# Kernel tuning notes

Measured on AMD Instinct MI355X. Metric: run time of the kernel, lower is better.

Reference implementation:

```python
import jax, jax.numpy as jnp
import numpy as np

B, NUM_FRAMES, NUM_PATCHES = 2, 16, 196
DIM, H, DH = 768, 12, 64
T = NUM_FRAMES * NUM_PATCHES  # 3136
EPS = 1e-5


def setup_inputs() -> dict:
    key = jax.random.key(0)
    ks = jax.random.split(key, 5)
    x = jax.random.normal(ks[0], (B, T, DIM), jnp.float32)
    context = jax.random.normal(ks[1], (B, T, DIM), jnp.float32)
    Wq = jax.random.normal(ks[2], (DIM, H * DH), jnp.float32) * 0.02
    Wkv = jax.random.normal(ks[3], (DIM, 2 * H * DH), jnp.float32) * 0.02
    Wo = jax.random.normal(ks[4], (H * DH, DIM), jnp.float32) * 0.02
    bo = jnp.zeros((DIM,), jnp.float32)
    gamma = jnp.ones((DIM,), jnp.float32)
    beta = jnp.zeros((DIM,), jnp.float32)
    # block-diagonal frame mask: patch i attends to patch j iff same frame
    frame_ids = jnp.arange(T) // NUM_PATCHES
    mask = frame_ids[:, None] == frame_ids[None, :]  # [T, T] bool
    return {"x": x, "context": context, "Wq": Wq, "Wkv": Wkv, "Wo": Wo,
            "bo": bo, "gamma": gamma, "beta": beta, "mask": mask}


def reference(x, context, Wq, Wkv, Wo, bo, gamma, beta, mask):
    # LayerNorm on queries only (torch LN: biased variance, eps=1e-5)
    mu = jnp.mean(x, axis=-1, keepdims=True)
    var = jnp.var(x, axis=-1, keepdims=True)
    xn = (x - mu) * jax.lax.rsqrt(var + EPS) * gamma + beta

    q = xn @ Wq                      # [B, T, H*DH]
    kv = context @ Wkv               # [B, T, 2*H*DH]
    k, v = jnp.split(kv, 2, axis=-1)

    def split_heads(t):
        return t.reshape(B, T, H, DH).transpose(0, 2, 1, 3)  # [B, H, T, DH]

    q, k, v = split_heads(q), split_heads(k), split_heads(v)

    scale = DH ** -0.5
    dots = jnp.einsum('bhnd,bhmd->bhnm', q, k) * scale      # [B, H, T, T]
    dots = jnp.where(mask, dots, -jnp.inf)
    attn = jax.nn.softmax(dots, axis=-1)                    # dropout p=0.0 -> identity
    out = jnp.einsum('bhnm,bhmd->bhnd', attn, v)            # [B, H, T, DH]
    out = out.transpose(0, 2, 1, 3).reshape(B, T, H * DH)
    return out @ Wo + bo
```

## Files before the change

### kernel.cpp

```cpp
#include <hip/hip_runtime.h>
#include <hip/hip_bf16.h>

#define NB 2
#define TT 3136
#define DIM 768
#define NH 12
#define NF 16
#define NP 196

typedef __attribute__((ext_vector_type(8))) short short8;
typedef __attribute__((ext_vector_type(4))) short s16x4;
typedef __attribute__((ext_vector_type(4))) float f32x4;
typedef unsigned int uint;

__device__ __forceinline__ float bf2f(short s) {
    return __uint_as_float(((uint)(unsigned short)s) << 16);
}
__device__ __forceinline__ short f2bs(float f) {
    __hip_bfloat16 h = __float2bfloat16(f);
    short s; __builtin_memcpy(&s, &h, 2); return s;
}
__device__ __forceinline__ uint pack2bf(float a, float b) {
    return (uint)(unsigned short)f2bs(a) | ((uint)(unsigned short)f2bs(b) << 16);
}
__device__ __forceinline__ void load16_lds(const void* g, void* l) {
    __builtin_amdgcn_global_load_lds(
        (const __attribute__((address_space(1))) unsigned int*)g,
        (__attribute__((address_space(3))) unsigned int*)l, 16, 0, 0);
}

__global__ __launch_bounds__(256)
void prep_all(const float* __restrict__ Wq, const float* __restrict__ Wkv,
              const float* __restrict__ Wo,
              __hip_bfloat16* __restrict__ WqT, __hip_bfloat16* __restrict__ WkvT,
              __hip_bfloat16* __restrict__ WoT,
              const float* __restrict__ ctx, __hip_bfloat16* __restrict__ cb,
              const float* __restrict__ x, const float* __restrict__ gamma,
              const float* __restrict__ beta, __hip_bfloat16* __restrict__ xn) {
    __shared__ float tile[32][33];
    int blk = blockIdx.x, tid = threadIdx.x;
    if (blk < 2304) {
        int bx = blk % 96, ky = blk / 96;
        const float* W; __hip_bfloat16* WT; int N, n0;
        if (bx < 24)      { W = Wq;  WT = WqT;  N = DIM;     n0 = bx * 32; }
        else if (bx < 72) { W = Wkv; WT = WkvT; N = 2 * DIM; n0 = (bx - 24) * 32; }
        else              { W = Wo;  WT = WoT;  N = DIM;     n0 = (bx - 72) * 32; }
        int k0 = ky * 32;
        int tx = tid & 31, ty = tid >> 5;
#pragma unroll
        for (int i = 0; i < 32; i += 8)
            tile[ty + i][tx] = W[(size_t)(k0 + ty + i) * N + (n0 + tx)];
        __syncthreads();
#pragma unroll
        for (int i = 0; i < 32; i += 8)
            WT[(size_t)(n0 + ty + i) * DIM + (k0 + tx)] = __float2bfloat16(tile[tx][ty + i]);
        return;
    }
    blk -= 2304;
    if (blk < 4704) {
        size_t i = (size_t)blk * 256 + tid;
        f32x4 f; __builtin_memcpy(&f, ctx + i * 4, 16);
        s16x4 s;
#pragma unroll
        for (int j = 0; j < 4; j++) s[j] = f2bs(f[j]);
        __builtin_memcpy((short*)cb + i * 4, &s, 8);
        return;
    }
    blk -= 4704;
    int wave = tid >> 6, lane = tid & 63;
    int row = blk * 4 + wave;
    const float* xr = x + (size_t)row * DIM;
    f32x4 v[3];
    float s = 0.f, ss = 0.f;
#pragma unroll
    for (int i = 0; i < 3; i++) {
        __builtin_memcpy(&v[i], xr + lane * 4 + i * 256, 16);
#pragma unroll
        for (int j = 0; j < 4; j++) { s += v[i][j]; ss += v[i][j] * v[i][j]; }
    }
#pragma unroll
    for (int off = 32; off; off >>= 1) {
        s += __shfl_xor(s, off);
        ss += __shfl_xor(ss, off);
    }
    float mu = s / DIM;
    float rs = rsqrtf(ss / DIM - mu * mu + 1e-5f);
#pragma unroll
    for (int i = 0; i < 3; i++) {
        int c = lane * 4 + i * 256;
        f32x4 g, bt;
        __builtin_memcpy(&g, gamma + c, 16);
        __builtin_memcpy(&bt, beta + c, 16);
        s16x4 o;
#pragma unroll
        for (int j = 0; j < 4; j++) o[j] = f2bs((v[i][j] - mu) * rs * g[j] + bt[j]);
        __builtin_memcpy((short*)xn + (size_t)row * DIM + c, &o, 8);
    }
}

__global__ __launch_bounds__(512, 1)
void gemm_qkv(const __hip_bfloat16* __restrict__ xn,
              const __hip_bfloat16* __restrict__ cb,
              const __hip_bfloat16* __restrict__ WqT,
              const __hip_bfloat16* __restrict__ WkvT,
              __hip_bfloat16* __restrict__ qbuf,
              __hip_bfloat16* __restrict__ kvbuf) {
    __shared__ short lds[3][24576];

    int orig = blockIdx.x;
    int xcd = orig & 7, pos = orig >> 3;
    int wgid = (xcd < 1 ? xcd * 56 : 56 + (xcd - 1) * 55) + pos;
    int mt = wgid / 9, nt = wgid - mt * 9;

    const __hip_bfloat16 *Abase, *Bbase; __hip_bfloat16* Cbase;
    int N, n0;
    if (nt < 3) { Abase = xn; Bbase = WqT;  Cbase = qbuf;  N = DIM;  n0 = nt * 256; }
    else        { Abase = cb; Bbase = WkvT; Cbase = kvbuf; N = 1536; n0 = (nt - 3) * 256; }
    int m0 = mt * 128;

    int tid = threadIdx.x, lane = tid & 63, wave = tid >> 6;
    int r = lane & 15, q = lane >> 4;
    int wm = wave >> 2, wn = wave & 3;
    f32x4 acc[4][4] = {};

    auto stageT = [&](int buf, int kt) {
        int k0 = kt * 64;
#pragma unroll
        for (int s = 0; s < 2; s++) {
            int idx = s * 512 + tid;
            int row = idx >> 3, cg = idx & 7;
            int w = (cg << 4) ^ ((row & 7) << 4);
            load16_lds((const char*)Abase + ((size_t)(m0 + row) * DIM + k0) * 2 + w,
                       (char*)&lds[buf][0] + idx * 16);
        }
#pragma unroll
        for (int h = 0; h < 2; h++)
#pragma unroll
            for (int s = 0; s < 2; s++) {
                int idx = s * 512 + tid;
                int row = idx >> 3, cg = idx & 7;
                int w = (cg << 4) ^ ((row & 7) << 4);
                load16_lds((const char*)Bbase + ((size_t)(n0 + h * 128 + row) * DIM + k0) * 2 + w,
                           (char*)&lds[buf][8192 + h * 8192] + idx * 16);
            }
    };

    auto read_frag = [&](const char* base, int frag_row, int ks) {
        short8 v;
        int byte_ = frag_row * 128 + ((ks * 64 + q * 16) ^ ((r & 7) << 4));
        __builtin_memcpy(&v, base + byte_, 16);
        return v;
    };

    auto compute = [&](int buf) {
        const char* Ab = (const char*)&lds[buf][0];
        const char* Bb = (const char*)&lds[buf][8192 + (wn >> 1) * 8192];
        int brow0 = (wn & 1) * 64;
        short8 af[4][2], bf[4][2];
#pragma unroll
        for (int m = 0; m < 4; m++)
#pragma unroll
            for (int ks = 0; ks < 2; ks++)
                af[m][ks] = read_frag(Ab, wm * 64 + m * 16 + r, ks);
#pragma unroll
        for (int n = 0; n < 4; n++)
#pragma unroll
            for (int ks = 0; ks < 2; ks++)
                bf[n][ks] = read_frag(Bb, brow0 + n * 16 + r, ks);
        __builtin_amdgcn_s_setprio(1);
#pragma unroll
        for (int m = 0; m < 4; m++)
#pragma unroll
            for (int n = 0; n < 4; n++)
#pragma unroll
                for (int ks = 0; ks < 2; ks++)
                    acc[m][n] = __builtin_amdgcn_mfma_f32_16x16x32_bf16(
                        af[m][ks], bf[n][ks], acc[m][n], 0, 0, 0);
        __builtin_amdgcn_s_setprio(0);
    };

    stageT(0, 0); stageT(1, 1);
    asm volatile("s_waitcnt vmcnt(6)" ::: "memory");
    __builtin_amdgcn_s_barrier();

    for (int t = 0; t < 12; ++t) {
        if (t < 10) stageT((t + 2) % 3, t + 2);
        compute(t % 3);
        if (t < 10)       asm volatile("s_waitcnt vmcnt(6)" ::: "memory");
        else if (t == 10) asm volatile("s_waitcnt vmcnt(0)" ::: "memory");
        if (t < 11) __builtin_amdgcn_s_barrier();
    }

#pragma unroll
    for (int m = 0; m < 4; m++)
#pragma unroll
        for (int n = 0; n < 4; n++)
#pragma unroll
            for (int rr = 0; rr < 4; rr++) {
                int row = m0 + wm * 64 + m * 16 + q * 4 + rr;
                int col = n0 + wn * 64 + n * 16 + r;
                Cbase[(size_t)row * N + col] = __float2bfloat16(acc[m][n][rr]);
            }
}

__global__ __launch_bounds__(256)
void gemm_o(const __hip_bfloat16* __restrict__ A,
            const __hip_bfloat16* __restrict__ BT,
            const float* __restrict__ bias,
            float* __restrict__ C) {
    __shared__ short sA[2][128 * 64];
    __shared__ short sB[2][128 * 64];
    int orig = blockIdx.x;
    int xcd = orig & 7, pos = orig >> 3;
    int wgid = (xcd < 6 ? xcd * 37 : 222 + (xcd - 6) * 36) + pos;
    int mt = wgid / 6, nt = wgid - mt * 6;
    int m0 = mt * 128, n0 = nt * 128;
    int tid = threadIdx.x, lane = tid & 63, wave = tid >> 6;
    int r = lane & 15, q = lane >> 4;
    int wm = (wave & 1) * 64, wn = (wave >> 1) * 64;
    f32x4 acc[4][4] = {};

    auto stage = [&](int buf, int k0) {
#pragma unroll
        for (int i = 0; i < 4; i++) {
            int c = i * 256 + tid;
            int row = c >> 3, cg = c & 7;
            load16_lds(A + (size_t)(m0 + row) * DIM + k0 + cg * 8, &sA[buf][c * 8]);
        }
#pragma unroll
        for (int i = 0; i < 4; i++) {
            int c = i * 256 + tid;
            int row = c >> 3, cg = c & 7;
            load16_lds(BT + (size_t)(n0 + row) * DIM + k0 + cg * 8, &sB[buf][c * 8]);
        }
    };
    auto compute = [&](int buf) {
#pragma unroll
        for (int ks = 0; ks < 2; ks++) {
            short8 af[4], bfv[4];
#pragma unroll
            for (int t = 0; t < 4; t++) {
                __builtin_memcpy(&af[t],  &sA[buf][(wm + t * 16 + r) * 64 + ks * 32 + q * 8], 16);
                __builtin_memcpy(&bfv[t], &sB[buf][(wn + t * 16 + r) * 64 + ks * 32 + q * 8], 16);
            }
            __builtin_amdgcn_s_setprio(1);
#pragma unroll
            for (int mi = 0; mi < 4; mi++)
#pragma unroll
                for (int ni = 0; ni < 4; ni++)
                    acc[mi][ni] = __builtin_amdgcn_mfma_f32_16x16x32_bf16(
                        af[mi], bfv[ni], acc[mi][ni], 0, 0, 0);
            __builtin_amdgcn_s_setprio(0);
        }
    };

    stage(0, 0);
    __syncthreads();
    int cur = 0;
#pragma unroll 2
    for (int t = 0; t < 11; ++t) {
        stage(cur ^ 1, (t + 1) * 64);
        compute(cur);
        __syncthreads();
        cur ^= 1;
    }
    compute(cur);

    float bv[4];
#pragma unroll
    for (int ni = 0; ni < 4; ni++) bv[ni] = bias[n0 + wn + ni * 16 + r];
#pragma unroll
    for (int mi = 0; mi < 4; mi++)
#pragma unroll
        for (int ni = 0; ni < 4; ni++)
#pragma unroll
            for (int rr = 0; rr < 4; rr++) {
                int row = m0 + wm + mi * 16 + q * 4 + rr;
                int col = n0 + wn + ni * 16 + r;
                C[(size_t)row * DIM + col] = acc[mi][ni][rr] + bv[ni];
            }
}

__global__ __launch_bounds__(448, 4)
void attn_kernel(__hip_bfloat16* qo,
                 const __hip_bfloat16* __restrict__ kvb) {
    __shared__ short sK[208 * 66];
    __shared__ short sVT[64 * 226];
    int blk = blockIdx.x;
    int f = blk % NF, h = (blk / NF) % NH, b = blk / (NF * NH);
    size_t tok0 = (size_t)b * TT + (size_t)f * NP;
    int tid = threadIdx.x, wave = tid >> 6, lane = tid & 63;
    int r = lane & 15, q = lane >> 4;

    short8 qf[2][2];
#pragma unroll
    for (int half = 0; half < 2; half++) {
        int qrow = half * 98 + wave * 16 + r;
        if (qrow >= NP) qrow = 0;
        const __hip_bfloat16* src = qo + (tok0 + qrow) * DIM + h * 64;
        __builtin_memcpy(&qf[half][0], src + q * 8, 16);
        __builtin_memcpy(&qf[half][1], src + 32 + q * 8, 16);
    }

    for (int e = tid; e < 1664; e += 448) {
        int row = e >> 3, cg = e & 7;
        short8 t = {0,0,0,0,0,0,0,0};
        if (row < NP)
            __builtin_memcpy(&t, kvb + (tok0 + row) * 1536 + h * 64 + cg * 8, 16);
        __builtin_memcpy(&sK[row * 66 + cg * 8], &t, 16);
    }
    for (int jj = 0; jj < 224; jj += 28) {
        int j = jj + (tid >> 4);
        int d = (tid & 15) * 4;
        s16x4 v = {0, 0, 0, 0};
        if (j < NP)
            __builtin_memcpy(&v, kvb + (tok0 + j) * 1536 + DIM + h * 64 + d, 8);
#pragma unroll
        for (int i = 0; i < 4; i++) sVT[(d + i) * 226 + j] = v[i];
    }
    __syncthreads();

#pragma unroll
    for (int half = 0; half < 2; half++) {
        int row0 = half * 98;

        f32x4 sacc[13];
#pragma unroll
        for (int jf = 0; jf < 13; jf++) {
            f32x4 a = {};
            short8 kf;
            __builtin_memcpy(&kf, &sK[(jf * 16 + r) * 66 + q * 8], 16);
            a = __builtin_amdgcn_mfma_f32_16x16x32_bf16(kf, qf[half][0], a, 0, 0, 0);
            __builtin_memcpy(&kf, &sK[(jf * 16 + r) * 66 + 32 + q * 8], 16);
            a = __builtin_amdgcn_mfma_f32_16x16x32_bf16(kf, qf[half][1], a, 0, 0, 0);
            sacc[jf] = a;
        }

        const float scale = 0.125f;
        float mx = -INFINITY;
#pragma unroll
        for (int jf = 0; jf < 13; jf++)
#pragma unroll
            for (int rg = 0; rg < 4; rg++) {
                bool valid = (jf < 12) | (q == 0);
                if (valid) mx = fmaxf(mx, sacc[jf][rg] * scale);
            }
        mx = fmaxf(mx, __shfl_xor(mx, 16));
        mx = fmaxf(mx, __shfl_xor(mx, 32));
        float ps = 0.f;
#pragma unroll
        for (int jf = 0; jf < 13; jf++)
#pragma unroll
            for (int rg = 0; rg < 4; rg++) {
                bool valid = (jf < 12) | (q == 0);
                float p = valid ? __expf(sacc[jf][rg] * scale - mx) : 0.f;
                sacc[jf][rg] = p;
                ps += p;
            }
        ps += __shfl_xor(ps, 16);
        ps += __shfl_xor(ps, 32);
        float inv = 1.f / ps;

        uint pk01[13], pk23[13];
#pragma unroll
        for (int jf = 0; jf < 13; jf++) {
            pk01[jf] = pack2bf(sacc[jf][0] * inv, sacc[jf][1] * inv);
            pk23[jf] = pack2bf(sacc[jf][2] * inv, sacc[jf][3] * inv);
        }
        int sl = (((2 * q) & 3) << 4) | r;
        int sh = (((2 * q + 1) & 3) << 4) | r;
        bool hiq = q >= 2;
        short8 pa[7];
#pragma unroll
        for (int c = 0; c < 7; c++) {
            uint a0 = (uint)__shfl((int)pk01[2 * c], sl, 64);
            uint a1 = (uint)__shfl((int)pk23[2 * c], sl, 64);
            uint a2 = (uint)__shfl((int)pk01[2 * c], sh, 64);
            uint a3 = (uint)__shfl((int)pk23[2 * c], sh, 64);
            uint b0 = 0, b1 = 0, b2 = 0, b3 = 0;
            if (c < 6) {
                b0 = (uint)__shfl((int)pk01[2 * c + 1], sl, 64);
                b1 = (uint)__shfl((int)pk23[2 * c + 1], sl, 64);
                b2 = (uint)__shfl((int)pk01[2 * c + 1], sh, 64);
                b3 = (uint)__shfl((int)pk23[2 * c + 1], sh, 64);
            }
            uint w[4] = { hiq ? b0 : a0, hiq ? b1 : a1, hiq ? b2 : a2, hiq ? b3 : a3 };
            __builtin_memcpy(&pa[c], w, 16);
        }

#pragma unroll
        for (int nt = 0; nt < 4; nt++) {
            f32x4 oacc = {};
#pragma unroll
            for (int kc = 0; kc < 7; kc++) {
                short8 bfv;
                __builtin_memcpy(&bfv, &sVT[(nt * 16 + r) * 226 + kc * 32 + q * 8], 16);
                oacc = __builtin_amdgcn_mfma_f32_16x16x32_bf16(pa[kc], bfv, oacc, 0, 0, 0);
            }
#pragma unroll
            for (int rg = 0; rg < 4; rg++) {
                int local = wave * 16 + q * 4 + rg;
                if (local < 98)
                    qo[(tok0 + row0 + local) * DIM + h * 64 + nt * 16 + r] =
                        __float2bfloat16(oacc[rg]);
            }
        }
    }
}

extern "C" void kernel_launch(void* const* d_in, const int* in_sizes, int n_in,
                              void* d_out, int out_size, void* d_ws, size_t ws_size,
                              hipStream_t stream) {
    const float* x     = (const float*)d_in[0];
    const float* ctx   = (const float*)d_in[1];
    const float* Wq    = (const float*)d_in[2];
    const float* Wkv   = (const float*)d_in[3];
    const float* Wo    = (const float*)d_in[4];
    const float* bo    = (const float*)d_in[5];
    const float* gamma = (const float*)d_in[6];
    const float* beta  = (const float*)d_in[7];

    char* ws = (char*)d_ws;
    __hip_bfloat16* cbuf  = (__hip_bfloat16*)(ws + 0);
    __hip_bfloat16* kvbuf = (__hip_bfloat16*)(ws + 9633792);
    __hip_bfloat16* qbuf  = (__hip_bfloat16*)(ws + 28901376);
    __hip_bfloat16* WqT   = (__hip_bfloat16*)(ws + 38535168);
    __hip_bfloat16* WkvT  = (__hip_bfloat16*)(ws + 39714816);
    __hip_bfloat16* WoT   = (__hip_bfloat16*)(ws + 42074112);
    __hip_bfloat16* xnbuf = (__hip_bfloat16*)d_out;
    float*          out   = (float*)d_out;

    prep_all<<<8576, 256, 0, stream>>>(Wq, Wkv, Wo, WqT, WkvT, WoT,
                                       ctx, cbuf, x, gamma, beta, xnbuf);
    gemm_qkv<<<441, 512, 0, stream>>>(xnbuf, cbuf, WqT, WkvT, qbuf, kvbuf);
    attn_kernel<<<NB * NH * NF, 448, 0, stream>>>(qbuf, kvbuf);
    gemm_o<<<294, 256, 0, stream>>>(qbuf, WoT, bo, out);
}
```

Measured before the change: 205.7 us.

## Fuse K/V projection into attention kernel and shrink QKV GEMM to Q-only

```diff
diff --git a/kernel.cpp b/kernel.cpp
--- a/kernel.cpp
+++ b/kernel.cpp
@@ -98,108 +98,77 @@
     }
 }
 
-__global__ __launch_bounds__(512, 1)
-void gemm_qkv(const __hip_bfloat16* __restrict__ xn,
-              const __hip_bfloat16* __restrict__ cb,
-              const __hip_bfloat16* __restrict__ WqT,
-              const __hip_bfloat16* __restrict__ WkvT,
-              __hip_bfloat16* __restrict__ qbuf,
-              __hip_bfloat16* __restrict__ kvbuf) {
-    __shared__ short lds[3][24576];
-
+__global__ __launch_bounds__(256)
+void gemm_q(const __hip_bfloat16* __restrict__ A,
+            const __hip_bfloat16* __restrict__ BT,
+            __hip_bfloat16* __restrict__ C) {
+    __shared__ short sA[2][128 * 64];
+    __shared__ short sB[2][128 * 64];
     int orig = blockIdx.x;
     int xcd = orig & 7, pos = orig >> 3;
-    int wgid = (xcd < 1 ? xcd * 56 : 56 + (xcd - 1) * 55) + pos;
-    int mt = wgid / 9, nt = wgid - mt * 9;
-
-    const __hip_bfloat16 *Abase, *Bbase; __hip_bfloat16* Cbase;
-    int N, n0;
-    if (nt < 3) { Abase = xn; Bbase = WqT;  Cbase = qbuf;  N = DIM;  n0 = nt * 256; }
-    else        { Abase = cb; Bbase = WkvT; Cbase = kvbuf; N = 1536; n0 = (nt - 3) * 256; }
-    int m0 = mt * 128;
-
+    int wgid = (xcd < 6 ? xcd * 37 : 222 + (xcd - 6) * 36) + pos;
+    int mt = wgid / 6, nt = wgid - mt * 6;
+    int m0 = mt * 128, n0 = nt * 128;
     int tid = threadIdx.x, lane = tid & 63, wave = tid >> 6;
     int r = lane & 15, q = lane >> 4;
-    int wm = wave >> 2, wn = wave & 3;
+    int wm = (wave & 1) * 64, wn = (wave >> 1) * 64;
     f32x4 acc[4][4] = {};
 
-    auto stageT = [&](int buf, int kt) {
-        int k0 = kt * 64;
-#pragma unroll
-        for (int s = 0; s < 2; s++) {
-            int idx = s * 512 + tid;
-            int row = idx >> 3, cg = idx & 7;
-            int w = (cg << 4) ^ ((row & 7) << 4);
-            load16_lds((const char*)Abase + ((size_t)(m0 + row) * DIM + k0) * 2 + w,
-                       (char*)&lds[buf][0] + idx * 16);
-        }
-#pragma unroll
-        for (int h = 0; h < 2; h++)
-#pragma unroll
-            for (int s = 0; s < 2; s++) {
-                int idx = s * 512 + tid;
-                int row = idx >> 3, cg = idx & 7;
-                int w = (cg << 4) ^ ((row & 7) << 4);
-                load16_lds((const char*)Bbase + ((size_t)(n0 + h * 128 + row) * DIM + k0) * 2 + w,
-                           (char*)&lds[buf][8192 + h * 8192] + idx * 16);
-            }
+    auto stage = [&](int buf, int k0) {
+#pragma unroll
+        for (int i = 0; i < 4; i++) {
+            int c = i * 256 + tid;
+            int row = c >> 3, cg = c & 7;
+            load16_lds(A + (size_t)(m0 + row) * DIM + k0 + cg * 8, &sA[buf][c * 8]);
+        }
+#pragma unroll
+        for (int i = 0; i < 4; i++) {
+            int c = i * 256 + tid;
+            int row = c >> 3, cg = c & 7;
+            load16_lds(BT + (size_t)(n0 + row) * DIM + k0 + cg * 8, &sB[buf][c * 8]);
+        }
     };
-
-    auto read_frag = [&](const char* base, int frag_row, int ks) {
-        short8 v;
-        int byte_ = frag_row * 128 + ((ks * 64 + q * 16) ^ ((r & 7) << 4));
-        __builtin_memcpy(&v, base + byte_, 16);
-        return v;
+    auto compute = [&](int buf) {
+#pragma unroll
+        for (int ks = 0; ks < 2; ks++) {
+            short8 af[4], bfv[4];
+#pragma unroll
+            for (int t = 0; t < 4; t++) {
+                __builtin_memcpy(&af[t],  &sA[buf][(wm + t * 16 + r) * 64 + ks * 32 + q * 8], 16);
+                __builtin_memcpy(&bfv[t], &sB[buf][(wn + t * 16 + r) * 64 + ks * 32 + q * 8], 16);
+            }
+            __builtin_amdgcn_s_setprio(1);
+#pragma unroll
+            for (int mi = 0; mi < 4; mi++)
+#pragma unroll
+                for (int ni = 0; ni < 4; ni++)
+                    acc[mi][ni] = __builtin_amdgcn_mfma_f32_16x16x32_bf16(
+                        af[mi], bfv[ni], acc[mi][ni], 0, 0, 0);
+            __builtin_amdgcn_s_setprio(0);
+        }
     };
 
-    auto compute = [&](int buf) {
-        const char* Ab = (const char*)&lds[buf][0];
-        const char* Bb = (const char*)&lds[buf][8192 + (wn >> 1) * 8192];
-        int brow0 = (wn & 1) * 64;
-        short8 af[4][2], bf[4][2];
-#pragma unroll
-        for (int m = 0; m < 4; m++)
-#pragma unroll
-            for (int ks = 0; ks < 2; ks++)
-                af[m][ks] = read_frag(Ab, wm * 64 + m * 16 + r, ks);
-#pragma unroll
-        for (int n = 0; n < 4; n++)
-#pragma unroll
-            for (int ks = 0; ks < 2; ks++)
-                bf[n][ks] = read_frag(Bb, brow0 + n * 16 + r, ks);
-        __builtin_amdgcn_s_setprio(1);
-#pragma unroll
-        for (int m = 0; m < 4; m++)
-#pragma unroll
-            for (int n = 0; n < 4; n++)
-#pragma unroll
-                for (int ks = 0; ks < 2; ks++)
-                    acc[m][n] = __builtin_amdgcn_mfma_f32_16x16x32_bf16(
-                        af[m][ks], bf[n][ks], acc[m][n], 0, 0, 0);
-        __builtin_amdgcn_s_setprio(0);
-    };
-
-    stageT(0, 0); stageT(1, 1);
-    asm volatile("s_waitcnt vmcnt(6)" ::: "memory");
-    __builtin_amdgcn_s_barrier();
-
-    for (int t = 0; t < 12; ++t) {
-        if (t < 10) stageT((t + 2) % 3, t + 2);
-        compute(t % 3);
-        if (t < 10)       asm volatile("s_waitcnt vmcnt(6)" ::: "memory");
-        else if (t == 10) asm volatile("s_waitcnt vmcnt(0)" ::: "memory");
-        if (t < 11) __builtin_amdgcn_s_barrier();
-    }
-
-#pragma unroll
-    for (int m = 0; m < 4; m++)
-#pragma unroll
-        for (int n = 0; n < 4; n++)
+    stage(0, 0);
+    __syncthreads();
+    int cur = 0;
+#pragma unroll 2
+    for (int t = 0; t < 11; ++t) {
+        stage(cur ^ 1, (t + 1) * 64);
+        compute(cur);
+        __syncthreads();
+        cur ^= 1;
+    }
+    compute(cur);
+
+#pragma unroll
+    for (int mi = 0; mi < 4; mi++)
+#pragma unroll
+        for (int ni = 0; ni < 4; ni++)
 #pragma unroll
             for (int rr = 0; rr < 4; rr++) {
-                int row = m0 + wm * 64 + m * 16 + q * 4 + rr;
-                int col = n0 + wn * 64 + n * 16 + r;
-                Cbase[(size_t)row * N + col] = __float2bfloat16(acc[m][n][rr]);
+                int row = m0 + wm + mi * 16 + q * 4 + rr;
+                int col = n0 + wn + ni * 16 + r;
+                C[(size_t)row * DIM + col] = __float2bfloat16(acc[mi][ni][rr]);
             }
 }
 
@@ -283,9 +252,13 @@
 
 __global__ __launch_bounds__(448, 4)
 void attn_kernel(__hip_bfloat16* qo,
-                 const __hip_bfloat16* __restrict__ kvb) {
-    __shared__ short sK[208 * 66];
-    __shared__ short sVT[64 * 226];
+                 const __hip_bfloat16* __restrict__ cb,
+                 const __hip_bfloat16* __restrict__ WkvT) {
+    __shared__ short smem[28192];
+    short* cbS = smem;
+    short* wS  = smem + 12544;
+    short* sK  = smem;
+    short* sVT = smem + 13728;
     int blk = blockIdx.x;
     int f = blk % NF, h = (blk / NF) % NH, b = blk / (NF * NH);
     size_t tok0 = (size_t)b * TT + (size_t)f * NP;
@@ -302,21 +275,69 @@
         __builtin_memcpy(&qf[half][1], src + 32 + q * 8, 16);
     }
 
-    for (int e = tid; e < 1664; e += 448) {
-        int row = e >> 3, cg = e & 7;
-        short8 t = {0,0,0,0,0,0,0,0};
-        if (row < NP)
-            __builtin_memcpy(&t, kvb + (tok0 + row) * 1536 + h * 64 + cg * 8, 16);
-        __builtin_memcpy(&sK[row * 66 + cg * 8], &t, 16);
-    }
-    for (int jj = 0; jj < 224; jj += 28) {
-        int j = jj + (tid >> 4);
-        int d = (tid & 15) * 4;
-        s16x4 v = {0, 0, 0, 0};
-        if (j < NP)
-            __builtin_memcpy(&v, kvb + (tok0 + j) * 1536 + DIM + h * 64 + d, 8);
-#pragma unroll
-        for (int i = 0; i < 4; i++) sVT[(d + i) * 226 + j] = v[i];
+    f32x4 acc0[8] = {}, acc1[8] = {};
+    for (int kc = 0; kc < 12; kc++) {
+        if (kc) __syncthreads();
+        int k0 = kc * 64;
+        for (int e = tid; e < 1568; e += 448) {
+            int row = e >> 3, cg = e & 7;
+            int sw = (cg ^ (row & 7)) << 4;
+            load16_lds((const char*)cb + ((size_t)(tok0 + row) * DIM + k0) * 2 + sw,
+                       (char*)cbS + e * 16);
+        }
+        for (int e = tid; e < 1024; e += 448) {
+            int row = e >> 3, cg = e & 7;
+            int sw = (cg ^ (row & 7)) << 4;
+            int wrow = (row < 64) ? (h * 64 + row) : (DIM + h * 64 + row - 64);
+            load16_lds((const char*)WkvT + ((size_t)wrow * DIM + k0) * 2 + sw,
+                       (char*)wS + e * 16);
+        }
+        __syncthreads();
+
+        short8 a0[2], a1[2];
+#pragma unroll
+        for (int ks = 0; ks < 2; ks++) {
+            int b0 = (2 * wave * 16 + r) * 128 + ((ks * 64 + q * 16) ^ ((r & 7) << 4));
+            int b1 = ((2 * wave + 1) * 16 + r) * 128 + ((ks * 64 + q * 16) ^ ((r & 7) << 4));
+            __builtin_memcpy(&a0[ks], (char*)cbS + b0, 16);
+            __builtin_memcpy(&a1[ks], (char*)cbS + b1, 16);
+        }
+        __builtin_amdgcn_s_setprio(1);
+#pragma unroll
+        for (int df = 0; df < 8; df++)
+#pragma unroll
+            for (int ks = 0; ks < 2; ks++) {
+                short8 bfv;
+                int bb = (df * 16 + r) * 128 + ((ks * 64 + q * 16) ^ ((r & 7) << 4));
+                __builtin_memcpy(&bfv, (char*)wS + bb, 16);
+                acc0[df] = __builtin_amdgcn_mfma_f32_16x16x32_bf16(a0[ks], bfv, acc0[df], 0, 0, 0);
+                acc1[df] = __builtin_amdgcn_mfma_f32_16x16x32_bf16(a1[ks], bfv, acc1[df], 0, 0, 0);
+            }
+        __builtin_amdgcn_s_setprio(0);
+    }
+    __syncthreads();
+
+#pragma unroll
+    for (int jj = 0; jj < 2; jj++)
+#pragma unroll
+        for (int df = 0; df < 8; df++)
+#pragma unroll
+            for (int i = 0; i < 4; i++) {
+                int j = (2 * wave + jj) * 16 + q * 4 + i;
+                if (j < NP) {
+                    float v = jj ? acc1[df][i] : acc0[df][i];
+                    short s = f2bs(v);
+                    if (df < 4) sK[j * 66 + df * 16 + r] = s;
+                    else        sVT[(df * 16 + r - 64) * 226 + j] = s;
+                }
+            }
+    for (int e = tid; e < 12 * 66; e += 448) {
+        int row = NP + e / 66, c = e % 66;
+        sK[row * 66 + c] = 0;
+    }
+    for (int e = tid; e < 64 * 30; e += 448) {
+        int d = e / 30, j = NP + e % 30;
+        sVT[d * 226 + j] = 0;
     }
     __syncthreads();
 
@@ -422,17 +443,16 @@
 
     char* ws = (char*)d_ws;
     __hip_bfloat16* cbuf  = (__hip_bfloat16*)(ws + 0);
-    __hip_bfloat16* kvbuf = (__hip_bfloat16*)(ws + 9633792);
-    __hip_bfloat16* qbuf  = (__hip_bfloat16*)(ws + 28901376);
-    __hip_bfloat16* WqT   = (__hip_bfloat16*)(ws + 38535168);
-    __hip_bfloat16* WkvT  = (__hip_bfloat16*)(ws + 39714816);
-    __hip_bfloat16* WoT   = (__hip_bfloat16*)(ws + 42074112);
+    __hip_bfloat16* qbuf  = (__hip_bfloat16*)(ws + 9633792);
+    __hip_bfloat16* WqT   = (__hip_bfloat16*)(ws + 19267584);
+    __hip_bfloat16* WkvT  = (__hip_bfloat16*)(ws + 20447232);
+    __hip_bfloat16* WoT   = (__hip_bfloat16*)(ws + 22806528);
     __hip_bfloat16* xnbuf = (__hip_bfloat16*)d_out;
     float*          out   = (float*)d_out;
 
     prep_all<<<8576, 256, 0, stream>>>(Wq, Wkv, Wo, WqT, WkvT, WoT,
                                        ctx, cbuf, x, gamma, beta, xnbuf);
-    gemm_qkv<<<441, 512, 0, stream>>>(xnbuf, cbuf, WqT, WkvT, qbuf, kvbuf);
-    attn_kernel<<<NB * NH * NF, 448, 0, stream>>>(qbuf, kvbuf);
+    gemm_q<<<294, 256, 0, stream>>>(xnbuf, WqT, qbuf);
+    attn_kernel<<<NB * NH * NF, 448, 0, stream>>>(qbuf, cbuf, WkvT);
     gemm_o<<<294, 256, 0, stream>>>(qbuf, WoT, bo, out);
 }
```

After: 203.6 us. Within noise of the previous version (-1.0%).
